# Kernel tuning notes

Hardware: AMD Instinct MI355X
Metric: run time of the kernel (lower is better)

Reference implementation:

```python
import jax, jax.numpy as jnp
import numpy as np

N_NODES = 50000
N_EDGES = 1600000
IN_DIM, HID_DIM, OUT_DIM, HEADS = 128, 128, 64, 8
NEG_SLOPE = 0.2
BN_EPS = 1e-5


def setup_inputs() -> dict:
    key = jax.random.key(0)
    ks = jax.random.split(key, 12)
    hpc = HID_DIM // HEADS  # per-head channels of layer 1
    return {
        "x": jax.random.normal(ks[0], (N_NODES, IN_DIM), jnp.float32),
        "edge_index": jax.random.randint(ks[1], (2, N_EDGES), 0, N_NODES, jnp.int64),
        "W1": jax.random.normal(ks[2], (IN_DIM, HEADS * hpc), jnp.float32) * 0.05,
        "a1_src": jax.random.normal(ks[3], (HEADS, hpc), jnp.float32) * 0.1,
        "a1_dst": jax.random.normal(ks[4], (HEADS, hpc), jnp.float32) * 0.1,
        "b1": jnp.zeros((HEADS * hpc,), jnp.float32),
        "bn_gamma": jnp.ones((HID_DIM,), jnp.float32),
        "bn_beta": jnp.zeros((HID_DIM,), jnp.float32),
        "W2": jax.random.normal(ks[5], (HID_DIM, OUT_DIM), jnp.float32) * 0.05,
        "a2_src": jax.random.normal(ks[6], (1, OUT_DIM), jnp.float32) * 0.1,
        "a2_dst": jax.random.normal(ks[7], (1, OUT_DIM), jnp.float32) * 0.1,
        "b2": jnp.zeros((OUT_DIM,), jnp.float32),
    }


def _gat_conv(x, src, dst, W, a_src, a_dst, bias, heads, n_nodes):
    # x: [N, Fin]; src/dst: [E'] (self-loops already appended)
    hpc = W.shape[1] // heads
    h = (x @ W).reshape(n_nodes, heads, hpc)                 # [N,H,C]
    alpha_s = jnp.einsum("nhc,hc->nh", h, a_src)             # [N,H]
    alpha_d = jnp.einsum("nhc,hc->nh", h, a_dst)
    e = alpha_s[src] + alpha_d[dst]                          # [E',H]
    e = jax.nn.leaky_relu(e, NEG_SLOPE)
    # segment softmax over destination neighborhoods
    m = jax.ops.segment_max(e, dst, num_segments=n_nodes)    # [N,H]
    m = jnp.where(jnp.isfinite(m), m, 0.0)
    ee = jnp.exp(e - m[dst])
    denom = jax.ops.segment_sum(ee, dst, num_segments=n_nodes)
    alpha = ee / (denom[dst] + 1e-16)                        # [E',H]
    msg = h[src] * alpha[:, :, None]                         # [E',H,C]
    out = jax.ops.segment_sum(msg, dst, num_segments=n_nodes)  # [N,H,C]
    return out.reshape(n_nodes, heads * hpc) + bias


def _batch_norm(x, gamma, beta):
    mu = jnp.mean(x, axis=0)
    var = jnp.var(x, axis=0)
    return gamma * (x - mu) * jax.lax.rsqrt(var + BN_EPS) + beta


def reference(x, edge_index, W1, a1_src, a1_dst, b1, bn_gamma, bn_beta, W2, a2_src, a2_dst, b2):
    n = x.shape[0]
    loops = jnp.arange(n, dtype=edge_index.dtype)
    src = jnp.concatenate([edge_index[0], loops])            # PyG add_self_loops
    dst = jnp.concatenate([edge_index[1], loops])
    h = _gat_conv(x, src, dst, W1, a1_src, a1_dst, b1, HEADS, n)
    h = _batch_norm(h, bn_gamma, bn_beta)
    h = jax.nn.elu(h)
    # dropout: identity at inference
    out = _gat_conv(h, src, dst, W2, a2_src, a2_dst, b2, 1, n)
    return out
```

## Files before the change

### kernel.cpp

```cpp
#include <hip/hip_runtime.h>
#include <hip/hip_bf16.h>

#define N_NODES 50000
#define N_EDGES 1600000
#define HEADS 8
#define NBK 196
#define NBLK 196
#define EPB 8192

typedef unsigned short u16;
typedef unsigned char u8;
typedef unsigned int u32;
typedef __attribute__((ext_vector_type(8))) short bf16x8;
typedef __attribute__((ext_vector_type(4))) float f32x4;

__device__ __forceinline__ float bf2f(u16 u) {
  union { u32 i; float f; } v; v.i = ((u32)u) << 16; return v.f;
}
__device__ __forceinline__ float bflo(u32 p) {
  union { u32 i; float f; } v; v.i = p << 16; return v.f;
}
__device__ __forceinline__ float bfhi(u32 p) {
  union { u32 i; float f; } v; v.i = p & 0xffff0000u; return v.f;
}
__device__ __forceinline__ u16 f2bf(float f) {
  union { float f; u32 i; } v; v.f = f;
  u32 r = v.i + 0x7fff + ((v.i >> 16) & 1);
  return (u16)(r >> 16);
}
__device__ __forceinline__ u32 pack2(float a, float b) {
  return (u32)f2bf(a) | ((u32)f2bf(b) << 16);
}

__global__ void k_detect(const u16* __restrict__ x, const u32* __restrict__ ei,
                         int* __restrict__ flags) {
  __shared__ int cbig, cnz;
  if (threadIdx.x == 0) { cbig = 0; cnz = 0; }
  __syncthreads();
  int lb = 0, ln = 0;
  for (int i = threadIdx.x; i < 4096; i += 256) {
    int ex = (x[i] >> 7) & 0xff;
    lb += (ex >= 140);
    if (i < 2048) ln += (ei[2 * i + 1] != 0);
  }
  atomicAdd(&cbig, lb); atomicAdd(&cnz, ln);
  __syncthreads();
  if (threadIdx.x == 0) {
    flags[0] = (cbig > 16) ? 1 : 0;
    flags[1] = (cnz == 0) ? 1 : 0;
  }
}

__global__ void k_convsmall(const void* a1s, const void* a1d, const void* b1,
                            const void* gam, const void* bet, const void* a2s,
                            const void* a2d, const void* b2, const void* W1,
                            const void* W2, float* __restrict__ smallf,
                            u16* __restrict__ w1t, u16* __restrict__ w2t,
                            const int* __restrict__ flags) {
  int i = blockIdx.x * 256 + threadIdx.x;
  if (i >= 25408) return;
  bool f32 = flags[0] != 0;
  auto ld = [&](const void* p, int off) -> float {
    return f32 ? ((const float*)p)[off] : bf2f(((const u16*)p)[off]);
  };
  if (i >= 17216) {
    int j = i - 17216, n = j >> 7, k = j & 127;
    w2t[j] = f2bf(ld(W2, k * 64 + n));
  } else if (i >= 832) {
    int j = i - 832, n = j >> 7, k = j & 127;
    w1t[j] = f2bf(ld(W1, k * 128 + n));
  } else {
    const void* src; int off;
    if (i >= 768)      { src = b2;  off = i - 768; }
    else if (i >= 704) { src = a2d; off = i - 704; }
    else if (i >= 640) { src = a2s; off = i - 640; }
    else if (i >= 512) { src = bet; off = i - 512; }
    else if (i >= 384) { src = gam; off = i - 384; }
    else if (i >= 256) { src = b1;  off = i - 256; }
    else if (i >= 128) { src = a1d; off = i - 128; }
    else               { src = a1s; off = i; }
    smallf[i] = ld(src, off);
  }
}

__global__ __launch_bounds__(256) void k_hist(const int* __restrict__ ei,
                                              int* __restrict__ H,
                                              int* __restrict__ totals,
                                              const int* __restrict__ flags) {
  __shared__ int hist[NBK];
  int t = threadIdx.x, blk = blockIdx.x;
  for (int i = t; i < NBK; i += 256) hist[i] = 0;
  __syncthreads();
  bool i64 = flags[1] != 0;
  int base = blk * EPB;
  for (int k = 0; k < 32; k++) {
    int e = base + k * 256 + t;
    if (e < N_EDGES) {
      int d = i64 ? ei[2 * (N_EDGES + e)] : ei[N_EDGES + e];
      atomicAdd(&hist[d >> 8], 1);
    }
  }
  __syncthreads();
  for (int i = t; i < NBK; i += 256) {
    H[i * NBLK + blk] = hist[i];
    atomicAdd(&totals[i], hist[i]);
  }
}

__global__ void k_scan_tot(const int* __restrict__ totals, int* __restrict__ bucketBase) {
  __shared__ int tmp[256];
  int t = threadIdx.x;
  int v = (t < NBK) ? totals[t] : 0;
  tmp[t] = v; __syncthreads();
  for (int o = 1; o < 256; o <<= 1) {
    int x = (t >= o) ? tmp[t - o] : 0; __syncthreads();
    tmp[t] += x; __syncthreads();
  }
  if (t < NBK) bucketBase[t] = tmp[t] - v;
  if (t == NBK - 1) bucketBase[NBK] = tmp[t];
}

__global__ void k_scan_blk(const int* __restrict__ H, const int* __restrict__ bucketBase,
                           int* __restrict__ P) {
  __shared__ int tmp[256];
  int t = threadIdx.x, b = blockIdx.x;
  int v = (t < NBLK) ? H[b * NBLK + t] : 0;
  tmp[t] = v; __syncthreads();
  for (int o = 1; o < 256; o <<= 1) {
    int x = (t >= o) ? tmp[t - o] : 0; __syncthreads();
    tmp[t] += x; __syncthreads();
  }
  if (t < NBLK) P[b * NBLK + t] = bucketBase[b] + tmp[t] - v;
}

__global__ __launch_bounds__(256) void k_bucket(const int* __restrict__ ei,
                                                const int* __restrict__ P,
                                                u32* __restrict__ buf,
                                                const int* __restrict__ flags) {
  __shared__ u32 sv[EPB];
  __shared__ u16 rank[EPB];
  __shared__ u8  sk8[EPB];
  __shared__ int cnt[NBK], scn[NBK], tmp[256];
  int t = threadIdx.x, blk = blockIdx.x;
  int base = blk * EPB;
  int nE = N_EDGES - base; if (nE > EPB) nE = EPB;
  for (int i = t; i < NBK; i += 256) cnt[i] = 0;
  __syncthreads();
  bool i64 = flags[1] != 0;
  for (int k = 0; k < EPB / 256; k++) {
    int li = k * 256 + t, e = base + li;
    if (li < nE) {
      int d = i64 ? ei[2 * (N_EDGES + e)] : ei[N_EDGES + e];
      rank[li] = (u16)atomicAdd(&cnt[d >> 8], 1);
    }
  }
  __syncthreads();
  int v = (t < NBK) ? cnt[t] : 0;
  tmp[t] = v; __syncthreads();
  for (int o = 1; o < 256; o <<= 1) {
    int x = (t >= o) ? tmp[t - o] : 0; __syncthreads();
    tmp[t] += x; __syncthreads();
  }
  if (t < NBK) scn[t] = tmp[t] - v;
  __syncthreads();
  for (int k = 0; k < EPB / 256; k++) {
    int li = k * 256 + t, e = base + li;
    if (li < nE) {
      int s = i64 ? ei[2 * e] : ei[e];
      int d = i64 ? ei[2 * (N_EDGES + e)] : ei[N_EDGES + e];
      int key = d >> 8;
      int pos = scn[key] + rank[li];
      sv[pos] = ((u32)(d & 255) << 16) | (u32)s;
      sk8[pos] = (u8)key;
    }
  }
  __syncthreads();
  for (int i = t; i < nE; i += 256) {
    int b = sk8[i];
    buf[P[b * NBLK + blk] + (i - scn[b])] = sv[i];
  }
}

__global__ __launch_bounds__(256) void k_csr(const u32* __restrict__ buf,
                                             const int* __restrict__ bucketBase,
                                             int* __restrict__ row_start,
                                             int* __restrict__ deg,
                                             int* __restrict__ csr, int N) {
  __shared__ int cnt[256], scn[256], cur[256];
  int b = blockIdx.x, t = threadIdx.x;
  int lo = bucketBase[b], hi = bucketBase[b + 1];
  cnt[t] = 0; __syncthreads();
  for (int e = lo + t; e < hi; e += 256) atomicAdd(&cnt[(buf[e] >> 16) & 255], 1);
  __syncthreads();
  int v = cnt[t];
  scn[t] = v; __syncthreads();
  for (int o = 1; o < 256; o <<= 1) {
    int x = (t >= o) ? scn[t - o] : 0; __syncthreads();
    scn[t] += x; __syncthreads();
  }
  int excl = scn[t] - v;
  int node = b * 256 + t;
  if (node < N) { row_start[node] = lo + excl; deg[node] = v; }
  cur[t] = lo + excl;
  __syncthreads();
  for (int e = lo + t; e < hi; e += 256) {
    u32 p = buf[e];
    int pos = atomicAdd(&cur[(p >> 16) & 255], 1);
    csr[pos] = p & 0xffff;
  }
}

template <int NCOLS, bool EPI, bool AFLAG>
__global__ __launch_bounds__(256) void k_gemm_mfma(const void* __restrict__ A,
                                                   const u16* __restrict__ BT,
                                                   const float* __restrict__ scale,
                                                   const float* __restrict__ shift,
                                                   const float* __restrict__ a2s,
                                                   const float* __restrict__ a2d,
                                                   float* __restrict__ as_out,
                                                   float* __restrict__ ad_out,
                                                   u16* __restrict__ C, int M,
                                                   const int* __restrict__ flags) {
  constexpr int KP = 136;
  constexpr int NT = NCOLS / 16;
  __shared__ u16 As[64 * KP];
  __shared__ u16 Bs[NCOLS * KP];
  int t = threadIdx.x;
  int row0 = blockIdx.x * 64;
  bool af32 = AFLAG ? (flags[0] != 0) : false;

  for (int i = t; i < NCOLS * 16; i += 256) {
    int n = i >> 4, q = i & 15;
    *(uint4*)&Bs[n * KP + q * 8] = ((const uint4*)BT)[n * 16 + q];
  }
  for (int i = t; i < 64 * 32; i += 256) {
    int r = i >> 5, c4 = i & 31;
    int row = row0 + r;
    uint2 pk = make_uint2(0u, 0u);
    if (row < M) {
      if (EPI) {
        uint2 p = ((const uint2*)A)[(size_t)row * 32 + c4];
        int c = c4 * 4;
        float v0 = bflo(p.x), v1 = bfhi(p.x), v2 = bflo(p.y), v3 = bfhi(p.y);
        v0 = fmaf(v0, scale[c],     shift[c]);     v0 = v0 > 0.f ? v0 : __expf(v0) - 1.f;
        v1 = fmaf(v1, scale[c + 1], shift[c + 1]); v1 = v1 > 0.f ? v1 : __expf(v1) - 1.f;
        v2 = fmaf(v2, scale[c + 2], shift[c + 2]); v2 = v2 > 0.f ? v2 : __expf(v2) - 1.f;
        v3 = fmaf(v3, scale[c + 3], shift[c + 3]); v3 = v3 > 0.f ? v3 : __expf(v3) - 1.f;
        pk.x = pack2(v0, v1); pk.y = pack2(v2, v3);
      } else if (af32) {
        float4 v = ((const float4*)A)[(size_t)row * 32 + c4];
        pk.x = pack2(v.x, v.y); pk.y = pack2(v.z, v.w);
      } else {
        pk = ((const uint2*)A)[(size_t)row * 32 + c4];
      }
    }
    *(uint2*)&As[r * KP + c4 * 4] = pk;
  }
  __syncthreads();

  int lane = t & 63, w = t >> 6;
  int m = lane & 15, quad = lane >> 4;
  f32x4 acc[NT];
#pragma unroll
  for (int nt = 0; nt < NT; nt++) acc[nt] = (f32x4)(0.f);
  const u16* aBase = &As[(w * 16 + m) * KP + quad * 8];
  const u16* bBase = &Bs[m * KP + quad * 8];
#pragma unroll
  for (int ks = 0; ks < 4; ks++) {
    bf16x8 af = *(const bf16x8*)(aBase + ks * 32);
#pragma unroll
    for (int nt = 0; nt < NT; nt++) {
      bf16x8 bf = *(const bf16x8*)(bBase + nt * 16 * KP + ks * 32);
      acc[nt] = __builtin_amdgcn_mfma_f32_16x16x32_bf16(af, bf, acc[nt], 0, 0, 0);
    }
  }
  int orow0 = row0 + w * 16 + quad * 4;
#pragma unroll
  for (int nt = 0; nt < NT; nt++) {
#pragma unroll
    for (int r = 0; r < 4; r++) {
      int row = orow0 + r;
      if (row < M) C[(size_t)row * NCOLS + nt * 16 + m] = f2bf(acc[nt][r]);
    }
  }
  if (EPI) {
    float a2sv[NT], a2dv[NT];
#pragma unroll
    for (int nt = 0; nt < NT; nt++) { a2sv[nt] = a2s[nt * 16 + m]; a2dv[nt] = a2d[nt * 16 + m]; }
#pragma unroll
    for (int r = 0; r < 4; r++) {
      float vs = 0.f, vd = 0.f;
#pragma unroll
      for (int nt = 0; nt < NT; nt++) {
        vs = fmaf(acc[nt][r], a2sv[nt], vs);
        vd = fmaf(acc[nt][r], a2dv[nt], vd);
      }
      vs += __shfl_xor(vs, 1); vd += __shfl_xor(vd, 1);
      vs += __shfl_xor(vs, 2); vd += __shfl_xor(vd, 2);
      vs += __shfl_xor(vs, 4); vd += __shfl_xor(vd, 4);
      vs += __shfl_xor(vs, 8); vd += __shfl_xor(vd, 8);
      int row = orow0 + r;
      if (row < M && m == 0) { as_out[row] = vs; ad_out[row] = vd; }
    }
  }
}

__global__ void k_alpha1(const u16* __restrict__ h1b, const float* __restrict__ a1s,
                         const float* __restrict__ a1d, float* __restrict__ as_out,
                         float* __restrict__ ad_out, int N) {
  int idx = blockIdx.x * 256 + threadIdx.x;
  if (idx >= N * HEADS) return;
  int n = idx >> 3, h = idx & 7;
  const u32* hp = (const u32*)&h1b[((size_t)n << 7) + (h << 4)];
  float s = 0.f, d = 0.f;
#pragma unroll
  for (int q = 0; q < 8; q++) {
    u32 p = hp[q];
    float v0 = bflo(p), v1 = bfhi(p);
    int b = (h << 4) + q * 2;
    s = fmaf(v0, a1s[b], s); s = fmaf(v1, a1s[b + 1], s);
    d = fmaf(v0, a1d[b], d); d = fmaf(v1, a1d[b + 1], d);
  }
  as_out[idx] = s; ad_out[idx] = d;
}

__global__ __launch_bounds__(256) void k_agg1(const u16* __restrict__ h1b,
                                              const float* __restrict__ as_,
                                              const float* __restrict__ ad_,
                                              const int* __restrict__ csr,
                                              const int* __restrict__ row_start,
                                              const int* __restrict__ deg,
                                              const float* __restrict__ b1,
                                              u16* __restrict__ out, int N) {
  int node = blockIdx.x * 4 + (threadIdx.x >> 6);
  if (node >= N) return;
  int l = threadIdx.x & 63;
  int head = l >> 3, sub = l & 7;
  int gbase = l & 56;
  int node_u = __builtin_amdgcn_readfirstlane(node);
  int st = __builtin_amdgcn_readfirstlane(row_start[node_u]);
  int cnt = __builtin_amdgcn_readfirstlane(deg[node_u]);
  const int* cp = csr + st;
  const u32* h32 = (const u32*)h1b;
  float ad = ad_[(node_u << 3) | head];
  float sp = 0.f, a0 = 0.f, a1 = 0.f;
  int j = 0;
  for (; j + 8 <= cnt; j += 8) {
    int ssub = cp[j + sub];
    float e = as_[(ssub << 3) | head] + ad;
    e = fmaxf(e, 0.2f * e);
    float p = __expf(e);
    sp += p;
#pragma unroll
    for (int k = 0; k < 8; k++) {
      int sk = cp[j + k];
      float pk = __shfl(p, gbase | k);
      u32 hv = h32[(sk << 6) | l];
      a0 = fmaf(pk, bflo(hv), a0);
      a1 = fmaf(pk, bfhi(hv), a1);
    }
  }
  for (; j < cnt; j++) {
    int s0 = cp[j];
    float e0 = as_[(s0 << 3) | head] + ad;
    e0 = fmaxf(e0, 0.2f * e0);
    float p0 = __expf(e0);
    if (sub == 0) sp += p0;
    u32 hv = h32[(s0 << 6) | l];
    a0 = fmaf(p0, bflo(hv), a0); a1 = fmaf(p0, bfhi(hv), a1);
  }
  {
    float e0 = as_[(node_u << 3) | head] + ad;
    e0 = fmaxf(e0, 0.2f * e0);
    float p0 = __expf(e0);
    if (sub == 0) sp += p0;
    u32 hv = h32[((size_t)node_u << 6) | l];
    a0 = fmaf(p0, bflo(hv), a0); a1 = fmaf(p0, bfhi(hv), a1);
  }
  sp += __shfl_xor(sp, 1);
  sp += __shfl_xor(sp, 2);
  sp += __shfl_xor(sp, 4);
  float inv = 1.f / (sp + 1e-16f);
  int c0 = l * 2;
  ((u32*)out)[((size_t)node_u << 6) + l] =
      pack2(fmaf(a0, inv, b1[c0]), fmaf(a1, inv, b1[c0 + 1]));
}

__global__ void k_bnstat(const u16* __restrict__ h, float* __restrict__ gsum,
                         float* __restrict__ gsq, int N) {
  __shared__ float ts[256], tq[256];
  int t = threadIdx.x, col = t & 127, rr = t >> 7;
  int row0 = blockIdx.x * 128;
  float s = 0.f, q = 0.f;
  for (int r = rr; r < 128; r += 2) {
    int row = row0 + r;
    if (row < N) {
      float v = bf2f(h[((size_t)row << 7) + col]);
      s += v; q = fmaf(v, v, q);
    }
  }
  ts[t] = s; tq[t] = q; __syncthreads();
  if (t < 128) {
    atomicAdd(&gsum[t], ts[t] + ts[t + 128]);
    atomicAdd(&gsq[t], tq[t] + tq[t + 128]);
  }
}

__global__ void k_bnfin(const float* __restrict__ gsum, const float* __restrict__ gsq,
                        const float* __restrict__ gamma, const float* __restrict__ beta,
                        float* __restrict__ scale, float* __restrict__ shift, int N) {
  int t = threadIdx.x;
  if (t >= 128) return;
  float mu = gsum[t] / (float)N;
  float var = fmaxf(gsq[t] / (float)N - mu * mu, 0.f);
  float s = gamma[t] * rsqrtf(var + 1e-5f);
  scale[t] = s;
  shift[t] = beta[t] - mu * s;
}

__global__ __launch_bounds__(256) void k_agg2(const u16* __restrict__ h2b,
                                              const float* __restrict__ as_,
                                              const float* __restrict__ ad_,
                                              const int* __restrict__ csr,
                                              const int* __restrict__ row_start,
                                              const int* __restrict__ deg,
                                              const float* __restrict__ b2,
                                              void* __restrict__ out,
                                              const int* __restrict__ flags, int N) {
  int node = blockIdx.x * 4 + (threadIdx.x >> 6);
  if (node >= N) return;
  int l = threadIdx.x & 63;
  int sub = l & 7, gbase = l & 56;
  int node_u = __builtin_amdgcn_readfirstlane(node);
  int st = __builtin_amdgcn_readfirstlane(row_start[node_u]);
  int cnt = __builtin_amdgcn_readfirstlane(deg[node_u]);
  const int* cp = csr + st;
  float ad = ad_[node_u];
  float sp = 0.f, a = 0.f;
  int j = 0;
  for (; j + 8 <= cnt; j += 8) {
    int ssub = cp[j + sub];
    float e = as_[ssub] + ad;
    e = fmaxf(e, 0.2f * e);
    float p = __expf(e);
    sp += p;
#pragma unroll
    for (int k = 0; k < 8; k++) {
      int sk = cp[j + k];
      float pk = __shfl(p, gbase | k);
      a = fmaf(pk, bf2f((h2b + (sk << 6))[l]), a);
    }
  }
  for (; j < cnt; j++) {
    int s0 = cp[j];
    float e0 = as_[s0] + ad;
    e0 = fmaxf(e0, 0.2f * e0);
    float p0 = __expf(e0);
    if (sub == 0) sp += p0;
    a = fmaf(p0, bf2f((h2b + (s0 << 6))[l]), a);
  }
  {
    float e0 = as_[node_u] + ad;
    e0 = fmaxf(e0, 0.2f * e0);
    float p0 = __expf(e0);
    if (sub == 0) sp += p0;
    a = fmaf(p0, bf2f((h2b + (node_u << 6))[l]), a);
  }
  sp += __shfl_xor(sp, 1);
  sp += __shfl_xor(sp, 2);
  sp += __shfl_xor(sp, 4);
  float r = a / (sp + 1e-16f) + b2[l];
  size_t idx = ((size_t)node_u << 6) + l;
  if (flags[0]) ((float*)out)[idx] = r;
  else          ((u16*)out)[idx] = f2bf(r);
}

extern "C" void kernel_launch(void* const* d_in, const int* in_sizes, int n_in,
                              void* d_out, int out_size, void* d_ws, size_t ws_size,
                              hipStream_t stream) {
  const void* x   = d_in[0];
  const int*  ei  = (const int*)d_in[1];
  const void* W1  = d_in[2];
  const void* a1s = d_in[3];
  const void* a1d = d_in[4];
  const void* b1  = d_in[5];
  const void* gam = d_in[6];
  const void* bet = d_in[7];
  const void* W2  = d_in[8];
  const void* a2s = d_in[9];
  const void* a2d = d_in[10];
  const void* b2  = d_in[11];

  char* ws = (char*)d_ws;
  size_t off = 0;
  auto alloc = [&](size_t bytes) -> void* {
    void* p = ws + off;
    off += (bytes + 255) & ~(size_t)255;
    return p;
  };
  int* flags = (int*)alloc(256);
  char* zreg = (char*)alloc(2048);
  int* totals = (int*)zreg;
  float* gsum = (float*)(zreg + 1024);
  float* gsq  = gsum + 128;
  int* H  = (int*)alloc((size_t)NBK * NBLK * 4);
  int* P  = (int*)alloc((size_t)NBK * NBLK * 4);
  int* bucketBase = (int*)alloc(1024);
  u32* ebuf = (u32*)alloc((size_t)N_EDGES * 4);
  int* csr = (int*)alloc((size_t)N_EDGES * 4);
  int* row_start = (int*)alloc((size_t)N_NODES * 4);
  int* deg = (int*)alloc((size_t)N_NODES * 4);
  float* smallf = (float*)alloc(832 * 4);
  float* a1sf = smallf;        float* a1df = smallf + 128;
  float* b1f  = smallf + 256;  float* gamf = smallf + 384;
  float* betf = smallf + 512;  float* a2sf = smallf + 640;
  float* a2df = smallf + 704;  float* b2f  = smallf + 768;
  u16* w1t = (u16*)alloc(16384 * 2);
  u16* w2t = (u16*)alloc(8192 * 2);
  u16* h1b  = (u16*)alloc((size_t)N_NODES * 128 * 2);
  u16* h1ob = (u16*)alloc((size_t)N_NODES * 128 * 2);
  u16* h2b  = (u16*)alloc((size_t)N_NODES * 64 * 2);
  float* al1s = (float*)alloc((size_t)N_NODES * 8 * 4);
  float* al1d = (float*)alloc((size_t)N_NODES * 8 * 4);
  float* scale = (float*)alloc(512);
  float* shift = (float*)alloc(512);
  float* al2s = (float*)alloc((size_t)N_NODES * 4);
  float* al2d = (float*)alloc((size_t)N_NODES * 4);
  if (off > ws_size) return;

  hipMemsetAsync(zreg, 0, 2048, stream);
  k_detect<<<1, 256, 0, stream>>>((const u16*)x, (const u32*)ei, flags);
  k_convsmall<<<100, 256, 0, stream>>>(a1s, a1d, b1, gam, bet, a2s, a2d, b2, W1, W2,
                                       smallf, w1t, w2t, flags);

  k_hist<<<NBLK, 256, 0, stream>>>(ei, H, totals, flags);
  k_scan_tot<<<1, 256, 0, stream>>>(totals, bucketBase);
  k_scan_blk<<<NBK, 256, 0, stream>>>(H, bucketBase, P);
  k_bucket<<<NBLK, 256, 0, stream>>>(ei, P, ebuf, flags);
  k_csr<<<NBK, 256, 0, stream>>>(ebuf, bucketBase, row_start, deg, csr, N_NODES);

  k_gemm_mfma<128, false, true><<<(N_NODES + 63) / 64, 256, 0, stream>>>(
      x, w1t, nullptr, nullptr, nullptr, nullptr, nullptr, nullptr, h1b, N_NODES, flags);
  k_alpha1<<<(N_NODES * HEADS + 255) / 256, 256, 0, stream>>>(h1b, a1sf, a1df,
                                                              al1s, al1d, N_NODES);
  k_agg1<<<(N_NODES + 3) / 4, 256, 0, stream>>>(h1b, al1s, al1d, csr, row_start, deg,
                                                b1f, h1ob, N_NODES);

  k_bnstat<<<(N_NODES + 127) / 128, 256, 0, stream>>>(h1ob, gsum, gsq, N_NODES);
  k_bnfin<<<1, 128, 0, stream>>>(gsum, gsq, gamf, betf, scale, shift, N_NODES);

  k_gemm_mfma<64, true, false><<<(N_NODES + 63) / 64, 256, 0, stream>>>(
      h1ob, w2t, scale, shift, a2sf, a2df, al2s, al2d, h2b, N_NODES, flags);
  k_agg2<<<(N_NODES + 3) / 4, 256, 0, stream>>>(h2b, al2s, al2d, csr, row_start, deg,
                                                b2f, d_out, flags, N_NODES);
}
```

Measured before the change: 329.1 us.

## Build CSR with global atomic counting sort and fuse layer-1 attention scores into GEMM

Replaces the two-level bucket sort (histogram, two scans, shared-memory bucketing, per-bucket CSR) with a direct counting sort. A global-atomic degree count is followed by a three-kernel prefix scan and an atomic-cursor fill that scatters source ids straight into the CSR array. It also removes the separate alpha1 kernel by computing per-head source and destination attention scores in the first GEMM's epilogue, using cross-lane shuffle reductions, so h1 is not re-read. The trade-off is contended global atomics and uncoalesced random scatter writes in place of the local-memory bucketing, and neighbour order inside each row becomes nondeterministic.

```diff
diff --git a/kernel.cpp b/kernel.cpp
--- a/kernel.cpp
+++ b/kernel.cpp
@@ -4,9 +4,6 @@
 #define N_NODES 50000
 #define N_EDGES 1600000
 #define HEADS 8
-#define NBK 196
-#define NBLK 196
-#define EPB 8192
 
 typedef unsigned short u16;
 typedef unsigned char u8;
@@ -83,134 +80,71 @@
   }
 }
 
-__global__ __launch_bounds__(256) void k_hist(const int* __restrict__ ei,
-                                              int* __restrict__ H,
-                                              int* __restrict__ totals,
-                                              const int* __restrict__ flags) {
-  __shared__ int hist[NBK];
-  int t = threadIdx.x, blk = blockIdx.x;
-  for (int i = t; i < NBK; i += 256) hist[i] = 0;
-  __syncthreads();
+__global__ __launch_bounds__(256) void k_deg(const int* __restrict__ ei,
+                                             int* __restrict__ deg,
+                                             const int* __restrict__ flags) {
   bool i64 = flags[1] != 0;
-  int base = blk * EPB;
-  for (int k = 0; k < 32; k++) {
-    int e = base + k * 256 + t;
-    if (e < N_EDGES) {
-      int d = i64 ? ei[2 * (N_EDGES + e)] : ei[N_EDGES + e];
-      atomicAdd(&hist[d >> 8], 1);
-    }
-  }
-  __syncthreads();
-  for (int i = t; i < NBK; i += 256) {
-    H[i * NBLK + blk] = hist[i];
-    atomicAdd(&totals[i], hist[i]);
-  }
-}
-
-__global__ void k_scan_tot(const int* __restrict__ totals, int* __restrict__ bucketBase) {
-  __shared__ int tmp[256];
-  int t = threadIdx.x;
-  int v = (t < NBK) ? totals[t] : 0;
+  int stride = gridDim.x * 256;
+  for (int e = blockIdx.x * 256 + threadIdx.x; e < N_EDGES; e += stride) {
+    int d = i64 ? ei[2 * (N_EDGES + e)] : ei[N_EDGES + e];
+    atomicAdd(&deg[d], 1);
+  }
+}
+
+__global__ __launch_bounds__(512) void k_scanA(const int* __restrict__ deg,
+                                               int* __restrict__ row_start,
+                                               int* __restrict__ bsum, int N) {
+  __shared__ int tmp[512];
+  int t = threadIdx.x, b = blockIdx.x;
+  int node = b * 512 + t;
+  int v = (node < N) ? deg[node] : 0;
   tmp[t] = v; __syncthreads();
-  for (int o = 1; o < 256; o <<= 1) {
+  for (int o = 1; o < 512; o <<= 1) {
     int x = (t >= o) ? tmp[t - o] : 0; __syncthreads();
     tmp[t] += x; __syncthreads();
   }
-  if (t < NBK) bucketBase[t] = tmp[t] - v;
-  if (t == NBK - 1) bucketBase[NBK] = tmp[t];
-}
-
-__global__ void k_scan_blk(const int* __restrict__ H, const int* __restrict__ bucketBase,
-                           int* __restrict__ P) {
-  __shared__ int tmp[256];
-  int t = threadIdx.x, b = blockIdx.x;
-  int v = (t < NBLK) ? H[b * NBLK + t] : 0;
+  if (node < N) row_start[node] = tmp[t] - v;
+  if (t == 511) bsum[b] = tmp[511];
+}
+
+__global__ void k_scanB(const int* __restrict__ bsum, int* __restrict__ bbase, int nb) {
+  __shared__ int tmp[128];
+  int t = threadIdx.x;
+  int v = (t < nb) ? bsum[t] : 0;
   tmp[t] = v; __syncthreads();
-  for (int o = 1; o < 256; o <<= 1) {
+  for (int o = 1; o < 128; o <<= 1) {
     int x = (t >= o) ? tmp[t - o] : 0; __syncthreads();
     tmp[t] += x; __syncthreads();
   }
-  if (t < NBLK) P[b * NBLK + t] = bucketBase[b] + tmp[t] - v;
-}
-
-__global__ __launch_bounds__(256) void k_bucket(const int* __restrict__ ei,
-                                                const int* __restrict__ P,
-                                                u32* __restrict__ buf,
-                                                const int* __restrict__ flags) {
-  __shared__ u32 sv[EPB];
-  __shared__ u16 rank[EPB];
-  __shared__ u8  sk8[EPB];
-  __shared__ int cnt[NBK], scn[NBK], tmp[256];
-  int t = threadIdx.x, blk = blockIdx.x;
-  int base = blk * EPB;
-  int nE = N_EDGES - base; if (nE > EPB) nE = EPB;
-  for (int i = t; i < NBK; i += 256) cnt[i] = 0;
-  __syncthreads();
+  if (t < nb) bbase[t] = tmp[t] - v;
+}
+
+__global__ __launch_bounds__(512) void k_scanC(int* __restrict__ row_start,
+                                               int* __restrict__ cur,
+                                               const int* __restrict__ bbase, int N) {
+  int node = blockIdx.x * 512 + threadIdx.x;
+  if (node < N) {
+    int r = row_start[node] + bbase[blockIdx.x];
+    row_start[node] = r;
+    cur[node] = r;
+  }
+}
+
+__global__ __launch_bounds__(256) void k_fill(const int* __restrict__ ei,
+                                              int* __restrict__ cur,
+                                              int* __restrict__ csr,
+                                              const int* __restrict__ flags) {
   bool i64 = flags[1] != 0;
-  for (int k = 0; k < EPB / 256; k++) {
-    int li = k * 256 + t, e = base + li;
-    if (li < nE) {
-      int d = i64 ? ei[2 * (N_EDGES + e)] : ei[N_EDGES + e];
-      rank[li] = (u16)atomicAdd(&cnt[d >> 8], 1);
-    }
-  }
-  __syncthreads();
-  int v = (t < NBK) ? cnt[t] : 0;
-  tmp[t] = v; __syncthreads();
-  for (int o = 1; o < 256; o <<= 1) {
-    int x = (t >= o) ? tmp[t - o] : 0; __syncthreads();
-    tmp[t] += x; __syncthreads();
-  }
-  if (t < NBK) scn[t] = tmp[t] - v;
-  __syncthreads();
-  for (int k = 0; k < EPB / 256; k++) {
-    int li = k * 256 + t, e = base + li;
-    if (li < nE) {
-      int s = i64 ? ei[2 * e] : ei[e];
-      int d = i64 ? ei[2 * (N_EDGES + e)] : ei[N_EDGES + e];
-      int key = d >> 8;
-      int pos = scn[key] + rank[li];
-      sv[pos] = ((u32)(d & 255) << 16) | (u32)s;
-      sk8[pos] = (u8)key;
-    }
-  }
-  __syncthreads();
-  for (int i = t; i < nE; i += 256) {
-    int b = sk8[i];
-    buf[P[b * NBLK + blk] + (i - scn[b])] = sv[i];
-  }
-}
-
-__global__ __launch_bounds__(256) void k_csr(const u32* __restrict__ buf,
-                                             const int* __restrict__ bucketBase,
-                                             int* __restrict__ row_start,
-                                             int* __restrict__ deg,
-                                             int* __restrict__ csr, int N) {
-  __shared__ int cnt[256], scn[256], cur[256];
-  int b = blockIdx.x, t = threadIdx.x;
-  int lo = bucketBase[b], hi = bucketBase[b + 1];
-  cnt[t] = 0; __syncthreads();
-  for (int e = lo + t; e < hi; e += 256) atomicAdd(&cnt[(buf[e] >> 16) & 255], 1);
-  __syncthreads();
-  int v = cnt[t];
-  scn[t] = v; __syncthreads();
-  for (int o = 1; o < 256; o <<= 1) {
-    int x = (t >= o) ? scn[t - o] : 0; __syncthreads();
-    scn[t] += x; __syncthreads();
-  }
-  int excl = scn[t] - v;
-  int node = b * 256 + t;
-  if (node < N) { row_start[node] = lo + excl; deg[node] = v; }
-  cur[t] = lo + excl;
-  __syncthreads();
-  for (int e = lo + t; e < hi; e += 256) {
-    u32 p = buf[e];
-    int pos = atomicAdd(&cur[(p >> 16) & 255], 1);
-    csr[pos] = p & 0xffff;
-  }
-}
-
-template <int NCOLS, bool EPI, bool AFLAG>
+  int stride = gridDim.x * 256;
+  for (int e = blockIdx.x * 256 + threadIdx.x; e < N_EDGES; e += stride) {
+    int s = i64 ? ei[2 * e] : ei[e];
+    int d = i64 ? ei[2 * (N_EDGES + e)] : ei[N_EDGES + e];
+    int pos = atomicAdd(&cur[d], 1);
+    csr[pos] = s;
+  }
+}
+
+template <int NCOLS, bool EPI, bool AFLAG, bool A1>
 __global__ __launch_bounds__(256) void k_gemm_mfma(const void* __restrict__ A,
                                                    const u16* __restrict__ BT,
                                                    const float* __restrict__ scale,
@@ -303,25 +237,28 @@
       if (row < M && m == 0) { as_out[row] = vs; ad_out[row] = vd; }
     }
   }
-}
-
-__global__ void k_alpha1(const u16* __restrict__ h1b, const float* __restrict__ a1s,
-                         const float* __restrict__ a1d, float* __restrict__ as_out,
-                         float* __restrict__ ad_out, int N) {
-  int idx = blockIdx.x * 256 + threadIdx.x;
-  if (idx >= N * HEADS) return;
-  int n = idx >> 3, h = idx & 7;
-  const u32* hp = (const u32*)&h1b[((size_t)n << 7) + (h << 4)];
-  float s = 0.f, d = 0.f;
-#pragma unroll
-  for (int q = 0; q < 8; q++) {
-    u32 p = hp[q];
-    float v0 = bflo(p), v1 = bfhi(p);
-    int b = (h << 4) + q * 2;
-    s = fmaf(v0, a1s[b], s); s = fmaf(v1, a1s[b + 1], s);
-    d = fmaf(v0, a1d[b], d); d = fmaf(v1, a1d[b + 1], d);
-  }
-  as_out[idx] = s; ad_out[idx] = d;
+  if (A1) {
+    float s1v[NT], d1v[NT];
+#pragma unroll
+    for (int nt = 0; nt < NT; nt++) { s1v[nt] = a2s[nt * 16 + m]; d1v[nt] = a2d[nt * 16 + m]; }
+#pragma unroll
+    for (int r = 0; r < 4; r++) {
+      int row = orow0 + r;
+#pragma unroll
+      for (int nt = 0; nt < NT; nt++) {
+        float vs = acc[nt][r] * s1v[nt];
+        float vd = acc[nt][r] * d1v[nt];
+        vs += __shfl_xor(vs, 1); vd += __shfl_xor(vd, 1);
+        vs += __shfl_xor(vs, 2); vd += __shfl_xor(vd, 2);
+        vs += __shfl_xor(vs, 4); vd += __shfl_xor(vd, 4);
+        vs += __shfl_xor(vs, 8); vd += __shfl_xor(vd, 8);
+        if (row < M && m == 0) {
+          as_out[(row << 3) | nt] = vs;
+          ad_out[(row << 3) | nt] = vd;
+        }
+      }
+    }
+  }
 }
 
 __global__ __launch_bounds__(256) void k_agg1(const u16* __restrict__ h1b,
@@ -499,17 +436,15 @@
     return p;
   };
   int* flags = (int*)alloc(256);
-  char* zreg = (char*)alloc(2048);
-  int* totals = (int*)zreg;
-  float* gsum = (float*)(zreg + 1024);
+  char* zreg = (char*)alloc(1024);
+  float* gsum = (float*)zreg;
   float* gsq  = gsum + 128;
-  int* H  = (int*)alloc((size_t)NBK * NBLK * 4);
-  int* P  = (int*)alloc((size_t)NBK * NBLK * 4);
-  int* bucketBase = (int*)alloc(1024);
-  u32* ebuf = (u32*)alloc((size_t)N_EDGES * 4);
-  int* csr = (int*)alloc((size_t)N_EDGES * 4);
   int* row_start = (int*)alloc((size_t)N_NODES * 4);
   int* deg = (int*)alloc((size_t)N_NODES * 4);
+  int* cur = (int*)alloc((size_t)N_NODES * 4);
+  int* bsum = (int*)alloc(512);
+  int* bbase = (int*)alloc(512);
+  int* csr = (int*)alloc(((size_t)N_EDGES + 64) * 4);
   float* smallf = (float*)alloc(832 * 4);
   float* a1sf = smallf;        float* a1df = smallf + 128;
   float* b1f  = smallf + 256;  float* gamf = smallf + 384;
@@ -528,28 +463,28 @@
   float* al2d = (float*)alloc((size_t)N_NODES * 4);
   if (off > ws_size) return;
 
-  hipMemsetAsync(zreg, 0, 2048, stream);
+  hipMemsetAsync(zreg, 0, 1024, stream);
+  hipMemsetAsync(deg, 0, (size_t)N_NODES * 4, stream);
   k_detect<<<1, 256, 0, stream>>>((const u16*)x, (const u32*)ei, flags);
   k_convsmall<<<100, 256, 0, stream>>>(a1s, a1d, b1, gam, bet, a2s, a2d, b2, W1, W2,
                                        smallf, w1t, w2t, flags);
 
-  k_hist<<<NBLK, 256, 0, stream>>>(ei, H, totals, flags);
-  k_scan_tot<<<1, 256, 0, stream>>>(totals, bucketBase);
-  k_scan_blk<<<NBK, 256, 0, stream>>>(H, bucketBase, P);
-  k_bucket<<<NBLK, 256, 0, stream>>>(ei, P, ebuf, flags);
-  k_csr<<<NBK, 256, 0, stream>>>(ebuf, bucketBase, row_start, deg, csr, N_NODES);
-
-  k_gemm_mfma<128, false, true><<<(N_NODES + 63) / 64, 256, 0, stream>>>(
-      x, w1t, nullptr, nullptr, nullptr, nullptr, nullptr, nullptr, h1b, N_NODES, flags);
-  k_alpha1<<<(N_NODES * HEADS + 255) / 256, 256, 0, stream>>>(h1b, a1sf, a1df,
-                                                              al1s, al1d, N_NODES);
+  k_deg<<<2048, 256, 0, stream>>>(ei, deg, flags);
+  int nscan = (N_NODES + 511) / 512;
+  k_scanA<<<nscan, 512, 0, stream>>>(deg, row_start, bsum, N_NODES);
+  k_scanB<<<1, 128, 0, stream>>>(bsum, bbase, nscan);
+  k_scanC<<<nscan, 512, 0, stream>>>(row_start, cur, bbase, N_NODES);
+  k_fill<<<2048, 256, 0, stream>>>(ei, cur, csr, flags);
+
+  k_gemm_mfma<128, false, true, true><<<(N_NODES + 63) / 64, 256, 0, stream>>>(
+      x, w1t, nullptr, nullptr, a1sf, a1df, al1s, al1d, h1b, N_NODES, flags);
   k_agg1<<<(N_NODES + 3) / 4, 256, 0, stream>>>(h1b, al1s, al1d, csr, row_start, deg,
                                                 b1f, h1ob, N_NODES);
 
   k_bnstat<<<(N_NODES + 127) / 128, 256, 0, stream>>>(h1ob, gsum, gsq, N_NODES);
   k_bnfin<<<1, 128, 0, stream>>>(gsum, gsq, gamf, betf, scale, shift, N_NODES);
 
-  k_gemm_mfma<64, true, false><<<(N_NODES + 63) / 64, 256, 0, stream>>>(
+  k_gemm_mfma<64, true, false, false><<<(N_NODES + 63) / 64, 256, 0, stream>>>(
       h1ob, w2t, scale, shift, a2sf, a2df, al2s, al2d, h2b, N_NODES, flags);
   k_agg2<<<(N_NODES + 3) / 4, 256, 0, stream>>>(h2b, al2s, al2d, csr, row_start, deg,
                                                 b2f, d_out, flags, N_NODES);
```

Measured after the change: 480.5 us. 46.0% more time.

## Fuse layer-1 attention logits into GEMM epilogue and split agg1 launch

Applied to the files above, without the earlier changes.

Removes the separate k_alpha1 kernel and computes the per-head source/destination attention scores inside the first MFMA GEMM's epilogue, using fp32 accumulators and shuffle reductions across the 16 columns of each head. This avoids re-reading h1b from memory and drops one launch. The agg1 kernel is now launched twice over the two halves of the nodes through a new base parameter, and the csr buffer gets 64 entries of padding. The epilogue computes scores from fp32 accumulators instead of bf16-rounded values, so results may differ slightly.

```diff
diff --git a/kernel.cpp b/kernel.cpp
--- a/kernel.cpp
+++ b/kernel.cpp
@@ -210,7 +210,7 @@
   }
 }
 
-template <int NCOLS, bool EPI, bool AFLAG>
+template <int NCOLS, bool EPI, bool AFLAG, bool A1>
 __global__ __launch_bounds__(256) void k_gemm_mfma(const void* __restrict__ A,
                                                    const u16* __restrict__ BT,
                                                    const float* __restrict__ scale,
@@ -303,25 +303,28 @@
       if (row < M && m == 0) { as_out[row] = vs; ad_out[row] = vd; }
     }
   }
-}
-
-__global__ void k_alpha1(const u16* __restrict__ h1b, const float* __restrict__ a1s,
-                         const float* __restrict__ a1d, float* __restrict__ as_out,
-                         float* __restrict__ ad_out, int N) {
-  int idx = blockIdx.x * 256 + threadIdx.x;
-  if (idx >= N * HEADS) return;
-  int n = idx >> 3, h = idx & 7;
-  const u32* hp = (const u32*)&h1b[((size_t)n << 7) + (h << 4)];
-  float s = 0.f, d = 0.f;
-#pragma unroll
-  for (int q = 0; q < 8; q++) {
-    u32 p = hp[q];
-    float v0 = bflo(p), v1 = bfhi(p);
-    int b = (h << 4) + q * 2;
-    s = fmaf(v0, a1s[b], s); s = fmaf(v1, a1s[b + 1], s);
-    d = fmaf(v0, a1d[b], d); d = fmaf(v1, a1d[b + 1], d);
-  }
-  as_out[idx] = s; ad_out[idx] = d;
+  if (A1) {
+    float s1v[NT], d1v[NT];
+#pragma unroll
+    for (int nt = 0; nt < NT; nt++) { s1v[nt] = a2s[nt * 16 + m]; d1v[nt] = a2d[nt * 16 + m]; }
+#pragma unroll
+    for (int r = 0; r < 4; r++) {
+      int row = orow0 + r;
+#pragma unroll
+      for (int nt = 0; nt < NT; nt++) {
+        float vs = acc[nt][r] * s1v[nt];
+        float vd = acc[nt][r] * d1v[nt];
+        vs += __shfl_xor(vs, 1); vd += __shfl_xor(vd, 1);
+        vs += __shfl_xor(vs, 2); vd += __shfl_xor(vd, 2);
+        vs += __shfl_xor(vs, 4); vd += __shfl_xor(vd, 4);
+        vs += __shfl_xor(vs, 8); vd += __shfl_xor(vd, 8);
+        if (row < M && m == 0) {
+          as_out[(row << 3) | nt] = vs;
+          ad_out[(row << 3) | nt] = vd;
+        }
+      }
+    }
+  }
 }
 
 __global__ __launch_bounds__(256) void k_agg1(const u16* __restrict__ h1b,
@@ -331,8 +334,8 @@
                                               const int* __restrict__ row_start,
                                               const int* __restrict__ deg,
                                               const float* __restrict__ b1,
-                                              u16* __restrict__ out, int N) {
-  int node = blockIdx.x * 4 + (threadIdx.x >> 6);
+                                              u16* __restrict__ out, int base, int N) {
+  int node = base + blockIdx.x * 4 + (threadIdx.x >> 6);
   if (node >= N) return;
   int l = threadIdx.x & 63;
   int head = l >> 3, sub = l & 7;
@@ -507,7 +510,7 @@
   int* P  = (int*)alloc((size_t)NBK * NBLK * 4);
   int* bucketBase = (int*)alloc(1024);
   u32* ebuf = (u32*)alloc((size_t)N_EDGES * 4);
-  int* csr = (int*)alloc((size_t)N_EDGES * 4);
+  int* csr = (int*)alloc(((size_t)N_EDGES + 64) * 4);
   int* row_start = (int*)alloc((size_t)N_NODES * 4);
   int* deg = (int*)alloc((size_t)N_NODES * 4);
   float* smallf = (float*)alloc(832 * 4);
@@ -539,17 +542,17 @@
   k_bucket<<<NBLK, 256, 0, stream>>>(ei, P, ebuf, flags);
   k_csr<<<NBK, 256, 0, stream>>>(ebuf, bucketBase, row_start, deg, csr, N_NODES);
 
-  k_gemm_mfma<128, false, true><<<(N_NODES + 63) / 64, 256, 0, stream>>>(
-      x, w1t, nullptr, nullptr, nullptr, nullptr, nullptr, nullptr, h1b, N_NODES, flags);
-  k_alpha1<<<(N_NODES * HEADS + 255) / 256, 256, 0, stream>>>(h1b, a1sf, a1df,
-                                                              al1s, al1d, N_NODES);
-  k_agg1<<<(N_NODES + 3) / 4, 256, 0, stream>>>(h1b, al1s, al1d, csr, row_start, deg,
-                                                b1f, h1ob, N_NODES);
+  k_gemm_mfma<128, false, true, true><<<(N_NODES + 63) / 64, 256, 0, stream>>>(
+      x, w1t, nullptr, nullptr, a1sf, a1df, al1s, al1d, h1b, N_NODES, flags);
+  k_agg1<<<6250, 256, 0, stream>>>(h1b, al1s, al1d, csr, row_start, deg,
+                                   b1f, h1ob, 0, 25000);
+  k_agg1<<<6250, 256, 0, stream>>>(h1b, al1s, al1d, csr, row_start, deg,
+                                   b1f, h1ob, 25000, N_NODES);
 
   k_bnstat<<<(N_NODES + 127) / 128, 256, 0, stream>>>(h1ob, gsum, gsq, N_NODES);
   k_bnfin<<<1, 128, 0, stream>>>(gsum, gsq, gamf, betf, scale, shift, N_NODES);
 
-  k_gemm_mfma<64, true, false><<<(N_NODES + 63) / 64, 256, 0, stream>>>(
+  k_gemm_mfma<64, true, false, false><<<(N_NODES + 63) / 64, 256, 0, stream>>>(
       h1ob, w2t, scale, shift, a2sf, a2df, al2s, al2d, h2b, N_NODES, flags);
   k_agg2<<<(N_NODES + 3) / 4, 256, 0, stream>>>(h2b, al2s, al2d, csr, row_start, deg,
                                                 b2f, d_out, flags, N_NODES);
```

New measurement: 346.1 us. 1.05x slower.
